# Kernel optimization log

Measured on AMD Instinct MI355X. Metric: run time of the kernel, lower is better.

Reference implementation:

```python
import jax, jax.numpy as jnp
import numpy as np

NUM_HEADS = 16
HEAD_DIM = 64  # hidden = 1024


def setup_inputs() -> dict:
    key = jax.random.key(0)
    k1, k2, k3 = jax.random.split(key, 3)
    B, S, Hd = 4, 4096, NUM_HEADS * HEAD_DIM
    x = jax.random.normal(k1, (B, S, Hd), dtype=jnp.float32)
    # xavier-uniform-ish scaling for the dense kernels
    Wqkv = jax.random.normal(k2, (Hd, 3 * Hd), dtype=jnp.float32) * (2.0 / (Hd + 3 * Hd)) ** 0.5
    bqkv = jnp.zeros((3 * Hd,), dtype=jnp.float32)
    Wout = jax.random.normal(k3, (Hd, Hd), dtype=jnp.float32) * (1.0 / Hd) ** 0.5
    bout = jnp.zeros((Hd,), dtype=jnp.float32)
    return {"x": x, "Wqkv": Wqkv, "bqkv": bqkv, "Wout": Wout, "bout": bout}


def reference(x, Wqkv, bqkv, Wout, bout):
    B, S, _ = x.shape
    H, D = NUM_HEADS, HEAD_DIM
    qkv = jnp.einsum('bsc,cf->bsf', x, Wqkv) + bqkv  # [B,S,3*H*D]
    q, k, v = jnp.split(qkv, 3, axis=-1)
    # source transposes to [B,H,S,D] before calling flax dot_product_attention_weights,
    # which interprets dims as [..., q_len=H, num_heads=S, depth=D]  (shape bug, kept faithfully)
    q = q.reshape(B, S, H, D).transpose(0, 2, 1, 3)  # [B,H,S,D]
    k = k.reshape(B, S, H, D).transpose(0, 2, 1, 3)
    v = v.reshape(B, S, H, D).transpose(0, 2, 1, 3)
    scale = D ** -0.5
    # flax: einsum('...qhd,...khd->...hqk') -> weights [B, S, H, H]
    logits = jnp.einsum('bqhd,bkhd->bhqk', q * scale, k)
    attn = jax.nn.softmax(logits, axis=-1)  # softmax over key-head axis
    # source: einsum('bhqk,bkhd->bqhd', weights, v) -> [B, H, S, D]
    out = jnp.einsum('bhqk,bkhd->bqhd', attn, v)
    out = out.transpose(0, 2, 1, 3).reshape(B, S, H * D)  # [B,S,hidden]
    return jnp.einsum('bsc,cf->bsf', out, Wout) + bout
```

## Files before the change

kernel.cpp:

```cpp
#include <hip/hip_runtime.h>
#include <hip/hip_bf16.h>

using bf16 = __hip_bfloat16;
typedef __bf16 bf16x8_t __attribute__((ext_vector_type(8)));
typedef float f32x4_t __attribute__((ext_vector_type(4)));

__device__ __forceinline__ void gl16(bf16* l, const bf16* g) {
  __builtin_amdgcn_global_load_lds(
      (const __attribute__((address_space(1))) unsigned int*)g,
      (__attribute__((address_space(3))) unsigned int*)l, 16, 0, 0);
}

#define BARRIER() do { asm volatile("" ::: "memory"); __builtin_amdgcn_s_barrier(); asm volatile("" ::: "memory"); } while (0)
#define WAITVM(N) asm volatile("s_waitcnt vmcnt(" #N ")" ::: "memory")

__global__ __launch_bounds__(256) void cvt_f32_bf16(const float* __restrict__ in,
                                                    bf16* __restrict__ out, int n4) {
  int i = blockIdx.x * 256 + threadIdx.x;
  if (i >= n4) return;
  float4 v = ((const float4*)in)[i];
  union { ushort4 u; bf16 b[4]; } o;
  o.b[0] = __float2bfloat16(v.x);
  o.b[1] = __float2bfloat16(v.y);
  o.b[2] = __float2bfloat16(v.z);
  o.b[3] = __float2bfloat16(v.w);
  ((ushort4*)out)[i] = o.u;
}

__global__ __launch_bounds__(256) void transpose_cvt(const float* __restrict__ in,
                                                     bf16* __restrict__ out, int R, int C) {
  __shared__ float t[32][33];
  int bx = blockIdx.x * 32, by = blockIdx.y * 32;
  int tx = threadIdx.x & 31, ty = threadIdx.x >> 5;
#pragma unroll
  for (int r = 0; r < 32; r += 8)
    t[ty + r][tx] = in[(size_t)(by + ty + r) * C + bx + tx];
  __syncthreads();
#pragma unroll
  for (int r = 0; r < 32; r += 8)
    out[(size_t)(bx + ty + r) * R + by + tx] = __float2bfloat16(t[tx][ty + r]);
}


template <int MH, int NH>
__device__ __forceinline__ void phase_loads(const bf16* lb, int wr, int wc, int lr, int lg, int exr,
                                            bf16x8_t (&af)[4][2], bf16x8_t (&bfr)[2][2]) {
  const bf16* ab = lb + MH * 8192;
  const bf16* bb = lb + (2 + NH) * 8192;
#pragma unroll
  for (int mi = 0; mi < 4; ++mi) {
    int R = wr * 64 + mi * 16 + lr;
    af[mi][0] = *(const bf16x8_t*)(ab + R * 64 + ((lg * 8) ^ exr));
    af[mi][1] = *(const bf16x8_t*)(ab + R * 64 + ((32 + lg * 8) ^ exr));
  }
#pragma unroll
  for (int ni = 0; ni < 2; ++ni) {
    int R = wc * 32 + ni * 16 + lr;
    bfr[ni][0] = *(const bf16x8_t*)(bb + R * 64 + ((lg * 8) ^ exr));
    bfr[ni][1] = *(const bf16x8_t*)(bb + R * 64 + ((32 + lg * 8) ^ exr));
  }
}

template <int MH, int NH>
__device__ __forceinline__ void phase_mfma(bf16x8_t (&af)[4][2], bf16x8_t (&bfr)[2][2],
                                           f32x4_t (&acc)[8][4]) {
  __builtin_amdgcn_s_setprio(1);
#pragma unroll
  for (int mi = 0; mi < 4; ++mi)
#pragma unroll
    for (int ni = 0; ni < 2; ++ni) {
      f32x4_t& a = acc[MH * 4 + mi][NH * 2 + ni];
      a = __builtin_amdgcn_mfma_f32_16x16x32_bf16(af[mi][0], bfr[ni][0], a, 0, 0, 0);
      a = __builtin_amdgcn_mfma_f32_16x16x32_bf16(af[mi][1], bfr[ni][1], a, 0, 0, 0);
    }
  __builtin_amdgcn_s_setprio(0);
}

#define DO_PHASE(BUF, MH, NH, STAGE, WAIT) do {                          \
    bf16x8_t af[4][2], bfr[2][2];                                        \
    phase_loads<MH, NH>(lds + (BUF) * 32768, wr, wc, lr, lg, exr, af, bfr); \
    STAGE; WAIT;                                                         \
    BARRIER();                                                           \
    phase_mfma<MH, NH>(af, bfr, acc);                                    \
    BARRIER();                                                           \
  } while (0)

template <int OUT_BF16>
__global__ __launch_bounds__(512, 2) void gemm256(const bf16* __restrict__ A,
                                                  const bf16* __restrict__ Bt,
                                                  const float* __restrict__ bias,
                                                  void* __restrict__ Cv,
                                                  int M, int N, int K) {
  __shared__ __align__(16) bf16 lds[65536];
  const int tid = threadIdx.x;
  const int nwgx = gridDim.x;
  int orig = blockIdx.y * nwgx + blockIdx.x;
  int cpx = (nwgx * gridDim.y) >> 3;
  int swzid = (orig & 7) * cpx + (orig >> 3);
  const int m0 = (swzid / nwgx) * 256, n0 = (swzid % nwgx) * 256;

  const int wid = tid >> 6, lane = tid & 63;
  const int wr = wid >> 2, wc = wid & 3;
  const int lr = lane & 15, lg = lane >> 4;
  const int exr = (lr & 7) << 3;

  const int srow = tid >> 3;
  const int colg = ((((tid & 7) * 16) ^ ((srow & 7) << 4)) >> 1);
  const int browc0 = (srow >> 5) * 64 + (srow & 31);

  auto stageA = [&](int b2, int h, int kt) {
    const bf16* g0 = A + (size_t)(m0 + h * 64 + srow) * K + kt * 64 + colg;
    const bf16* g1 = A + (size_t)(m0 + 128 + h * 64 + srow) * K + kt * 64 + colg;
    bf16* l = lds + b2 * 32768 + h * 8192 + tid * 8;
    gl16(l, g0); gl16(l + 4096, g1);
  };
  auto stageB = [&](int b2, int h, int kt) {
    const bf16* g0 = Bt + (size_t)(n0 + browc0 + h * 32) * K + kt * 64 + colg;
    const bf16* g1 = Bt + (size_t)(n0 + 128 + browc0 + h * 32) * K + kt * 64 + colg;
    bf16* l = lds + b2 * 32768 + (2 + h) * 8192 + tid * 8;
    gl16(l, g0); gl16(l + 4096, g1);
  };

  f32x4_t acc[8][4] = {};
  const int nt = K >> 6;

  stageA(0, 0, 0); stageB(0, 0, 0); stageA(0, 1, 0); stageB(0, 1, 0);
  stageA(1, 0, 1); stageB(1, 0, 1);
  WAITVM(4);
  BARRIER();

  for (int t = 0; t <= nt - 3; ++t) {
    const int buf = t & 1, bufn = buf ^ 1;
    DO_PHASE(buf, 0, 0, stageA(bufn, 1, t + 1), (void)0);
    DO_PHASE(buf, 0, 1, stageB(bufn, 1, t + 1), (void)0);
    DO_PHASE(buf, 1, 0, stageA(buf, 0, t + 2), (void)0);
    DO_PHASE(buf, 1, 1, stageB(buf, 0, t + 2), WAITVM(4));
  }
  {
    const int t = nt - 2;
    const int buf = t & 1, bufn = buf ^ 1;
    DO_PHASE(buf, 0, 0, stageA(bufn, 1, t + 1), (void)0);
    DO_PHASE(buf, 0, 1, stageB(bufn, 1, t + 1), (void)0);
    DO_PHASE(buf, 1, 0, (void)0, (void)0);
    DO_PHASE(buf, 1, 1, (void)0, WAITVM(0));
  }
  {
    const int buf = (nt - 1) & 1;
    DO_PHASE(buf, 0, 0, (void)0, (void)0);
    DO_PHASE(buf, 0, 1, (void)0, (void)0);
    DO_PHASE(buf, 1, 0, (void)0, (void)0);
    DO_PHASE(buf, 1, 1, (void)0, (void)0);
  }

#pragma unroll
  for (int n = 0; n < 4; ++n) {
    int col = n0 + wc * 64 + n * 16 + lr;
    float bv = bias[col];
#pragma unroll
    for (int m = 0; m < 8; ++m) {
      int row = m0 + wr * 128 + m * 16 + lg * 4;
#pragma unroll
      for (int j = 0; j < 4; ++j) {
        float v = acc[m][n][j] + bv;
        if (OUT_BF16)
          ((bf16*)Cv)[(size_t)(row + j) * N + col] = __float2bfloat16(v);
        else
          ((float*)Cv)[(size_t)(row + j) * N + col] = v;
      }
    }
  }
}

#define PSTR 48
__global__ __launch_bounds__(256) void attn_tok(const bf16* __restrict__ qkv,
                                                bf16* __restrict__ out) {
  __shared__ __align__(16) bf16 vs[4][1024];
  __shared__ __align__(16) bf16 ps[4][16 * PSTR];
  const int w = threadIdx.x >> 6, l = threadIdx.x & 63;
  const int t = blockIdx.x * 4 + w;
  const int lr = l & 15, lg = l >> 4;
  const bf16* base = qkv + (size_t)t * 3072;

  bf16x8_t v0 = *(const bf16x8_t*)(base + 2048 + l * 16);
  bf16x8_t v1 = *(const bf16x8_t*)(base + 2048 + l * 16 + 8);
  *(bf16x8_t*)(&vs[w][l * 16]) = v0;
  *(bf16x8_t*)(&vs[w][l * 16 + 8]) = v1;

  *(unsigned long long*)(&ps[w][(l >> 2) * PSTR + 16 + (l & 3) * 4]) = 0ULL;

  const bf16* qp = base + lr * 64 + lg * 8;
  const bf16* kp = base + 1024 + lr * 64 + lg * 8;
  bf16x8_t qa0 = *(const bf16x8_t*)qp;
  bf16x8_t ka0 = *(const bf16x8_t*)kp;
  bf16x8_t qa1 = *(const bf16x8_t*)(qp + 32);
  bf16x8_t ka1 = *(const bf16x8_t*)(kp + 32);
  f32x4_t s = {};
  s = __builtin_amdgcn_mfma_f32_16x16x32_bf16(qa0, ka0, s, 0, 0, 0);
  s = __builtin_amdgcn_mfma_f32_16x16x32_bf16(qa1, ka1, s, 0, 0, 0);

#pragma unroll
  for (int j = 0; j < 4; ++j) {
    float x = s[j] * 0.125f;
    float mx = x;
#pragma unroll
    for (int off = 8; off; off >>= 1) mx = fmaxf(mx, __shfl_xor(mx, off, 16));
    float e = __expf(x - mx);
    float sum = e;
#pragma unroll
    for (int off = 8; off; off >>= 1) sum += __shfl_xor(sum, off, 16);
    ps[w][(lg * 4 + j) * PSTR + lr] = __float2bfloat16(e / sum);
  }

  bf16x8_t pf = *(const bf16x8_t*)(&ps[w][lr * PSTR + lg * 8]);
  bf16x8_t vf[4] = {};
  if (l < 32) {
#pragma unroll
    for (int c = 0; c < 4; ++c)
#pragma unroll
      for (int j = 0; j < 8; ++j)
        vf[c][j] = (__bf16)vs[w][(lg * 8 + j) * 64 + c * 16 + lr];
  }
  f32x4_t o[4] = {};
#pragma unroll
  for (int c = 0; c < 4; ++c)
    o[c] = __builtin_amdgcn_mfma_f32_16x16x32_bf16(pf, vf[c], o[c], 0, 0, 0);

  bf16* ob = out + (size_t)t * 1024;
#pragma unroll
  for (int c = 0; c < 4; ++c)
#pragma unroll
    for (int j = 0; j < 4; ++j)
      ob[(lg * 4 + j) * 64 + c * 16 + lr] = __float2bfloat16(o[c][j]);
}

extern "C" void kernel_launch(void* const* d_in, const int* in_sizes, int n_in,
                              void* d_out, int out_size, void* d_ws, size_t ws_size,
                              hipStream_t stream) {
  const float* x    = (const float*)d_in[0];
  const float* Wqkv = (const float*)d_in[1];
  const float* bqkv = (const float*)d_in[2];
  const float* Wout = (const float*)d_in[3];
  const float* bout = (const float*)d_in[4];
  float* y = (float*)d_out;

  const int T = 16384, HD = 1024, N1 = 3072;

  char* ws = (char*)d_ws;
  size_t off = 0;
  bf16* xb  = (bf16*)(ws + off); off += (size_t)T * HD * 2;
  bf16* w1t = (bf16*)(ws + off); off += (size_t)N1 * HD * 2;
  bf16* w2t = (bf16*)(ws + off); off += (size_t)HD * HD * 2;
  bf16* qkv = (bf16*)(ws + off); off += (size_t)T * N1 * 2;
  if (ws_size < off) return;
  bf16* ao = xb;

  cvt_f32_bf16<<<(T * HD / 4 + 255) / 256, 256, 0, stream>>>(x, xb, T * HD / 4);
  transpose_cvt<<<dim3(N1 / 32, HD / 32), 256, 0, stream>>>(Wqkv, w1t, HD, N1);
  transpose_cvt<<<dim3(HD / 32, HD / 32), 256, 0, stream>>>(Wout, w2t, HD, HD);

  gemm256<1><<<dim3(N1 / 256, T / 256), 512, 0, stream>>>(xb, w1t, bqkv, qkv, T, N1, HD);
  attn_tok<<<T / 4, 256, 0, stream>>>(qkv, ao);
  gemm256<0><<<dim3(HD / 256, T / 256), 512, 0, stream>>>(ao, w2t, bout, y, T, HD, HD);
}
```

Measured before the change: 220.1 us.

## Make GEMMs persistent with cross-tile prefetch pipeline over 256 workgroups

After: 219.5 us. About the same (-0.3%).

```diff
diff --git a/kernel.cpp b/kernel.cpp
--- a/kernel.cpp
+++ b/kernel.cpp
@@ -85,19 +85,20 @@
     BARRIER();                                                           \
   } while (0)
 
-template <int OUT_BF16>
-__global__ __launch_bounds__(512, 2) void gemm256(const bf16* __restrict__ A,
-                                                  const bf16* __restrict__ Bt,
-                                                  const float* __restrict__ bias,
-                                                  void* __restrict__ Cv,
-                                                  int M, int N, int K) {
+template <int OUT_BF16, int NWGX>
+__global__ __launch_bounds__(512, 2) void gemm256p(const bf16* __restrict__ A,
+                                                   const bf16* __restrict__ Bt,
+                                                   const float* __restrict__ bias,
+                                                   void* __restrict__ Cv) {
+  constexpr int K = 1024;
+  constexpr int N = NWGX * 256;
+  constexpr int TT = NWGX / 4;
+  constexpr int G = TT * 16;
+  constexpr int CPX = NWGX * 8;
+
   __shared__ __align__(16) bf16 lds[65536];
   const int tid = threadIdx.x;
-  const int nwgx = gridDim.x;
-  int orig = blockIdx.y * nwgx + blockIdx.x;
-  int cpx = (nwgx * gridDim.y) >> 3;
-  int swzid = (orig & 7) * cpx + (orig >> 3);
-  const int m0 = (swzid / nwgx) * 256, n0 = (swzid % nwgx) * 256;
+  const int bx = blockIdx.x;
 
   const int wid = tid >> 6, lane = tid & 63;
   const int wr = wid >> 2, wc = wid & 3;
@@ -108,64 +109,66 @@
   const int colg = ((((tid & 7) * 16) ^ ((srow & 7) << 4)) >> 1);
   const int browc0 = (srow >> 5) * 64 + (srow & 31);
 
-  auto stageA = [&](int b2, int h, int kt) {
-    const bf16* g0 = A + (size_t)(m0 + h * 64 + srow) * K + kt * 64 + colg;
-    const bf16* g1 = A + (size_t)(m0 + 128 + h * 64 + srow) * K + kt * 64 + colg;
-    bf16* l = lds + b2 * 32768 + h * 8192 + tid * 8;
-    gl16(l, g0); gl16(l + 4096, g1);
+  auto tileMN = [&](int tt, int& m0, int& n0) {
+    int orig = bx + (tt << 8);
+    int swz = (orig & 7) * CPX + (orig >> 3);
+    m0 = (swz / NWGX) * 256;
+    n0 = (swz % NWGX) * 256;
   };
-  auto stageB = [&](int b2, int h, int kt) {
-    const bf16* g0 = Bt + (size_t)(n0 + browc0 + h * 32) * K + kt * 64 + colg;
-    const bf16* g1 = Bt + (size_t)(n0 + 128 + browc0 + h * 32) * K + kt * 64 + colg;
-    bf16* l = lds + b2 * 32768 + (2 + h) * 8192 + tid * 8;
-    gl16(l, g0); gl16(l + 4096, g1);
+
+  auto stageA = [&](int g, int h) {
+    if (g >= G) return;
+    int m0, n0; tileMN(g >> 4, m0, n0);
+    const bf16* g0 = A + (size_t)(m0 + h * 64 + srow) * K + (g & 15) * 64 + colg;
+    bf16* l = lds + (g & 1) * 32768 + h * 8192 + tid * 8;
+    gl16(l, g0); gl16(l + 4096, g0 + (size_t)128 * K);
   };
+  auto stageB = [&](int g, int h) {
+    if (g >= G) return;
+    int m0, n0; tileMN(g >> 4, m0, n0);
+    const bf16* g0 = Bt + (size_t)(n0 + browc0 + h * 32) * K + (g & 15) * 64 + colg;
+    bf16* l = lds + (g & 1) * 32768 + (2 + h) * 8192 + tid * 8;
+    gl16(l, g0); gl16(l + 4096, g0 + (size_t)128 * K);
+  };
 
   f32x4_t acc[8][4] = {};
-  const int nt = K >> 6;
-
-  stageA(0, 0, 0); stageB(0, 0, 0); stageA(0, 1, 0); stageB(0, 1, 0);
-  stageA(1, 0, 1); stageB(1, 0, 1);
+
+  stageA(0, 0); stageB(0, 0); stageA(0, 1); stageB(0, 1);
+  stageA(1, 0); stageB(1, 0);
   WAITVM(4);
   BARRIER();
 
-  for (int t = 0; t <= nt - 3; ++t) {
-    const int buf = t & 1, bufn = buf ^ 1;
-    DO_PHASE(buf, 0, 0, stageA(bufn, 1, t + 1), (void)0);
-    DO_PHASE(buf, 0, 1, stageB(bufn, 1, t + 1), (void)0);
-    DO_PHASE(buf, 1, 0, stageA(buf, 0, t + 2), (void)0);
-    DO_PHASE(buf, 1, 1, stageB(buf, 0, t + 2), WAITVM(4));
-  }
-  {
-    const int t = nt - 2;
-    const int buf = t & 1, bufn = buf ^ 1;
-    DO_PHASE(buf, 0, 0, stageA(bufn, 1, t + 1), (void)0);
-    DO_PHASE(buf, 0, 1, stageB(bufn, 1, t + 1), (void)0);
-    DO_PHASE(buf, 1, 0, (void)0, (void)0);
-    DO_PHASE(buf, 1, 1, (void)0, WAITVM(0));
-  }
-  {
-    const int buf = (nt - 1) & 1;
-    DO_PHASE(buf, 0, 0, (void)0, (void)0);
-    DO_PHASE(buf, 0, 1, (void)0, (void)0);
-    DO_PHASE(buf, 1, 0, (void)0, (void)0);
-    DO_PHASE(buf, 1, 1, (void)0, (void)0);
-  }
-
-#pragma unroll
-  for (int n = 0; n < 4; ++n) {
-    int col = n0 + wc * 64 + n * 16 + lr;
-    float bv = bias[col];
-#pragma unroll
-    for (int m = 0; m < 8; ++m) {
-      int row = m0 + wr * 128 + m * 16 + lg * 4;
-#pragma unroll
-      for (int j = 0; j < 4; ++j) {
-        float v = acc[m][n][j] + bv;
-        if (OUT_BF16)
-          ((bf16*)Cv)[(size_t)(row + j) * N + col] = __float2bfloat16(v);
-        else
-          ((float*)Cv)[(size_t)(row + j) * N + col] = v;
+  for (int g = 0; g < G; ++g) {
+    const int buf = g & 1;
+    DO_PHASE(buf, 0, 0, stageA(g + 1, 1), (void)0);
+    DO_PHASE(buf, 0, 1, stageB(g + 1, 1), (void)0);
+    DO_PHASE(buf, 1, 0, stageA(g + 2, 0), (void)0);
+    if (g < G - 2) {
+      DO_PHASE(buf, 1, 1, stageB(g + 2, 0), WAITVM(4));
+    } else if (g == G - 2) {
+      DO_PHASE(buf, 1, 1, (void)0, WAITVM(0));
+    } else {
+      DO_PHASE(buf, 1, 1, (void)0, (void)0);
+    }
+
+    if ((g & 15) == 15) {
+      int m0, n0; tileMN(g >> 4, m0, n0);
+#pragma unroll
+      for (int m = 0; m < 8; ++m) {
+        int row = m0 + wr * 128 + m * 16 + lg * 4;
+#pragma unroll
+        for (int j = 0; j < 4; ++j) {
+#pragma unroll
+          for (int n = 0; n < 4; ++n) {
+            int col = n0 + wc * 64 + n * 16 + lr;
+            float v = acc[m][n][j] + bias[col];
+            if (OUT_BF16)
+              ((bf16*)Cv)[(size_t)(row + j) * N + col] = __float2bfloat16(v);
+            else
+              ((float*)Cv)[(size_t)(row + j) * N + col] = v;
+            acc[m][n][j] = 0.f;
+          }
+        }
       }
     }
   }
@@ -258,7 +261,7 @@
   transpose_cvt<<<dim3(N1 / 32, HD / 32), 256, 0, stream>>>(Wqkv, w1t, HD, N1);
   transpose_cvt<<<dim3(HD / 32, HD / 32), 256, 0, stream>>>(Wout, w2t, HD, HD);
 
-  gemm256<1><<<dim3(N1 / 256, T / 256), 512, 0, stream>>>(xb, w1t, bqkv, qkv, T, N1, HD);
+  gemm256p<1, 12><<<256, 512, 0, stream>>>(xb, w1t, bqkv, qkv);
   attn_tok<<<T / 4, 256, 0, stream>>>(qkv, ao);
-  gemm256<0><<<dim3(HD / 256, T / 256), 512, 0, stream>>>(ao, w2t, bout, y, T, HD, HD);
-}
+  gemm256p<0, 4><<<256, 512, 0, stream>>>(ao, w2t, bout, y);
+}
```
